# Optimization experiments

Hardware: AMD Instinct MI355X
Metric: run time of the kernel (lower is better)

The kernel has to match this reference:

```python
import jax, jax.numpy as jnp
import numpy as np

D_MODEL = 1024
N_HEADS = 16
D_K = D_MODEL // N_HEADS


def setup_inputs() -> dict:
    key = jax.random.key(0)
    ks = jax.random.split(key, 11)
    B, S = 2, 2048
    scale = 1.0 / np.sqrt(D_MODEL)
    inp = {
        "q": jax.random.normal(ks[0], (B, S, D_MODEL), jnp.float32),
        "k": jax.random.normal(ks[1], (B, S, D_MODEL), jnp.float32),
        "v": jax.random.normal(ks[2], (B, S, D_MODEL), jnp.float32),
        "W_q": jax.random.normal(ks[3], (D_MODEL, D_MODEL), jnp.float32) * scale,
        "b_q": jnp.zeros((D_MODEL,), jnp.float32),
        "W_k": jax.random.normal(ks[4], (D_MODEL, D_MODEL), jnp.float32) * scale,
        "b_k": jnp.zeros((D_MODEL,), jnp.float32),
        "W_v": jax.random.normal(ks[5], (D_MODEL, D_MODEL), jnp.float32) * scale,
        "b_v": jnp.zeros((D_MODEL,), jnp.float32),
        "W_o": jax.random.normal(ks[6], (D_MODEL, D_MODEL), jnp.float32) * scale,
        "b_o": jnp.zeros((D_MODEL,), jnp.float32),
    }
    return inp


def _split_heads(x):
    B, S, _ = x.shape
    return x.reshape(B, S, N_HEADS, D_K).transpose(0, 2, 1, 3)  # [B,H,S,dk]


def reference(q, k, v, W_q, b_q, W_k, b_k, W_v, b_v, W_o, b_o):
    Q = _split_heads(q @ W_q + b_q)
    K = _split_heads(k @ W_k + b_k)
    V = _split_heads(v @ W_v + b_v)
    scores = jnp.einsum("bhqd,bhkd->bhqk", Q, K) / jnp.sqrt(jnp.float32(D_K))
    attn = jax.nn.softmax(scores, axis=-1)  # [B,H,S,S]
    out = jnp.einsum("bhqk,bhkd->bhqd", attn, V)
    B, H, S, dk = out.shape
    out = out.transpose(0, 2, 1, 3).reshape(B, S, H * dk)
    return out @ W_o + b_o, attn
```

## Files before the change

### kernel.cpp

```cpp
#include <hip/hip_runtime.h>
#include <hip/hip_bf16.h>

typedef __bf16 bf16x8 __attribute__((ext_vector_type(8)));
typedef float f32x4 __attribute__((ext_vector_type(4)));
typedef short short4v __attribute__((ext_vector_type(4)));
typedef unsigned short ushort8v __attribute__((ext_vector_type(8)));

#define DEV static __device__ __forceinline__

#if __has_builtin(__builtin_amdgcn_exp2f)
#define EXP2(x) __builtin_amdgcn_exp2f(x)
#else
#define EXP2(x) exp2f(x)
#endif

DEV unsigned short f2bf(float x) {
  union { __hip_bfloat16 b; unsigned short u; } c;
  c.b = __float2bfloat16(x);
  return c.u;
}

DEV unsigned short f2bf_fast(float x) {
  union { float f; unsigned u; } c;
  c.f = x;
  unsigned u = c.u + 0x7fff + ((c.u >> 16) & 1);
  return (unsigned short)(u >> 16);
}

DEV void gload_lds16(const void* g, void* l) {
  __builtin_amdgcn_global_load_lds((const __attribute__((address_space(1))) void*)g,
                                   (__attribute__((address_space(3))) void*)l, 16, 0, 0);
}

__global__ __launch_bounds__(256) void cvt_qkv(const float* __restrict__ q,
                                               const float* __restrict__ k,
                                               const float* __restrict__ v,
                                               unsigned short* __restrict__ qb,
                                               unsigned short* __restrict__ kb,
                                               unsigned short* __restrict__ vb) {
  const float* src = blockIdx.y == 0 ? q : (blockIdx.y == 1 ? k : v);
  unsigned short* dst = blockIdx.y == 0 ? qb : (blockIdx.y == 1 ? kb : vb);
  int idx = (blockIdx.x * 256 + threadIdx.x) * 4;
  float4 xv = *(const float4*)(src + idx);
  ushort4 o;
  o.x = f2bf(xv.x); o.y = f2bf(xv.y); o.z = f2bf(xv.z); o.w = f2bf(xv.w);
  *(ushort4*)(dst + idx) = o;
}

__global__ __launch_bounds__(256) void transpose_all(const float* __restrict__ W0,
                                                     const float* __restrict__ W1,
                                                     const float* __restrict__ W2,
                                                     const float* __restrict__ W3,
                                                     unsigned short* __restrict__ T0,
                                                     unsigned short* __restrict__ T1,
                                                     unsigned short* __restrict__ T2,
                                                     unsigned short* __restrict__ T3) {
  __shared__ float t[64][68];
  int sel = blockIdx.x >> 8;
  const float* W = sel == 0 ? W0 : sel == 1 ? W1 : sel == 2 ? W2 : W3;
  unsigned short* Wt = sel == 0 ? T0 : sel == 1 ? T1 : sel == 2 ? T2 : T3;
  int tile = blockIdx.x & 255;
  int tr = tile >> 4, tc = tile & 15;
  int lr = threadIdx.x >> 4, lc4 = threadIdx.x & 15;
#pragma unroll
  for (int i = 0; i < 4; ++i) {
    int r = i * 16 + lr;
    float4 v = *(const float4*)(W + (size_t)(tr * 64 + r) * 1024 + tc * 64 + lc4 * 4);
    t[r][lc4 * 4 + 0] = v.x; t[r][lc4 * 4 + 1] = v.y;
    t[r][lc4 * 4 + 2] = v.z; t[r][lc4 * 4 + 3] = v.w;
  }
  __syncthreads();
#pragma unroll
  for (int i = 0; i < 4; ++i) {
    int r = i * 16 + lr;
    ushort4 o;
    o.x = f2bf(t[lc4 * 4 + 0][r]);
    o.y = f2bf(t[lc4 * 4 + 1][r]);
    o.z = f2bf(t[lc4 * 4 + 2][r]);
    o.w = f2bf(t[lc4 * 4 + 3][r]);
    *(ushort4*)(Wt + (size_t)(tc * 64 + r) * 1024 + tr * 64 + lc4 * 4) = o;
  }
}

DEV void gemm_core(const unsigned short* __restrict__ A, const unsigned short* __restrict__ Bt,
                   const float* __restrict__ bias, void* __restrict__ Cout,
                   float scale, int mode, int blk,
                   unsigned short* As, unsigned short* Bs) {
  const int tid = threadIdx.x;
  const int l = tid & 63, w = tid >> 6;
  const int wm = w >> 1, wn = w & 1;
  const int r15 = l & 15, kg = l >> 4;
  const int mt = blk >> 3, nt = blk & 7;

  const f32x4 fz = {0.f, 0.f, 0.f, 0.f};
  f32x4 acc[4][4];
#pragma unroll
  for (int i = 0; i < 4; ++i)
#pragma unroll
    for (int j = 0; j < 4; ++j) acc[i][j] = fz;

  for (int kt = 0; kt < 16; ++kt) {
#pragma unroll
    for (int c = 0; c < 4; ++c) {
      int chunk = c * 256 + tid;
      int row = chunk >> 3, slot = chunk & 7;
      int gsl = slot ^ (row & 7);
      gload_lds16(A + (size_t)(mt * 128 + row) * 1024 + kt * 64 + gsl * 8, As + chunk * 8);
      gload_lds16(Bt + (size_t)(nt * 128 + row) * 1024 + kt * 64 + gsl * 8, Bs + chunk * 8);
    }
    __syncthreads();
#pragma unroll
    for (int ks = 0; ks < 2; ++ks) {
      bf16x8 a[4], b[4];
      int slot = ks * 4 + kg;
#pragma unroll
      for (int i = 0; i < 4; ++i) {
        int ra = wm * 64 + i * 16 + r15;
        a[i] = *(const bf16x8*)(As + ra * 64 + (slot ^ (ra & 7)) * 8);
        int rb = wn * 64 + i * 16 + r15;
        b[i] = *(const bf16x8*)(Bs + rb * 64 + (slot ^ (rb & 7)) * 8);
      }
#pragma unroll
      for (int i = 0; i < 4; ++i)
#pragma unroll
        for (int j = 0; j < 4; ++j)
          acc[i][j] = __builtin_amdgcn_mfma_f32_16x16x32_bf16(a[i], b[j], acc[i][j], 0, 0, 0);
    }
    __syncthreads();
  }

#pragma unroll
  for (int j = 0; j < 4; ++j) {
    int gc = nt * 128 + wn * 64 + j * 16 + r15;
    float bj = bias[gc];
#pragma unroll
    for (int i = 0; i < 4; ++i) {
#pragma unroll
      for (int r = 0; r < 4; ++r) {
        int gr = mt * 128 + wm * 64 + i * 16 + kg * 4 + r;
        float val = (acc[i][j][r] + bj) * scale;
        if (mode == 2) {
          ((float*)Cout)[(size_t)gr * 1024 + gc] = val;
        } else {
          int bb = gr >> 11, s = gr & 2047, hh = gc >> 6, dk = gc & 63;
          if (mode == 0)
            ((unsigned short*)Cout)[((size_t)(bb * 16 + hh) * 2048 + s) * 64 + dk] = f2bf(val);
          else
            ((unsigned short*)Cout)[((size_t)(bb * 16 + hh) * 64 + dk) * 2048 + s] = f2bf(val);
        }
      }
    }
  }
}

__global__ __launch_bounds__(256) void gemm_qkv(const unsigned short* __restrict__ qb,
                                                const unsigned short* __restrict__ kb,
                                                const unsigned short* __restrict__ vb,
                                                const unsigned short* __restrict__ Wtq,
                                                const unsigned short* __restrict__ Wtk,
                                                const unsigned short* __restrict__ Wtv,
                                                const float* __restrict__ bq,
                                                const float* __restrict__ bk,
                                                const float* __restrict__ bv,
                                                unsigned short* __restrict__ Qh,
                                                unsigned short* __restrict__ Kh,
                                                unsigned short* __restrict__ Vt) {
  __shared__ unsigned short As[128 * 64];
  __shared__ unsigned short Bs[128 * 64];
  int sel = blockIdx.x >> 8, blk = blockIdx.x & 255;
  const unsigned short* A = sel == 0 ? qb : sel == 1 ? kb : vb;
  const unsigned short* Bt = sel == 0 ? Wtq : sel == 1 ? Wtk : Wtv;
  const float* bias = sel == 0 ? bq : sel == 1 ? bk : bv;
  void* C = sel == 0 ? (void*)Qh : sel == 1 ? (void*)Kh : (void*)Vt;
  gemm_core(A, Bt, bias, C, sel == 0 ? 0.125f * 1.44269504088896f : 1.0f,
            sel == 2 ? 1 : 0, blk, As, Bs);
}

__global__ __launch_bounds__(256) void gemm_out(const unsigned short* __restrict__ AO,
                                                const unsigned short* __restrict__ Wto,
                                                const float* __restrict__ bo,
                                                float* __restrict__ out0) {
  __shared__ unsigned short As[128 * 64];
  __shared__ unsigned short Bs[128 * 64];
  gemm_core(AO, Wto, bo, out0, 1.0f, 2, blockIdx.x, As, Bs);
}

__global__ __launch_bounds__(256) void attn_flash(const unsigned short* __restrict__ Qh,
                                                  const unsigned short* __restrict__ Kh,
                                                  const unsigned short* __restrict__ Vt,
                                                  unsigned short* __restrict__ AO,
                                                  float* __restrict__ rrowG) {
  __shared__ float Ored[4][32][68];
  __shared__ float Ss[4][32];
  __shared__ float rrow[32];

  const int tid = threadIdx.x;
  const int l = tid & 63, w = tid >> 6;
  const int r15 = l & 15, kg = l >> 4;

  const int lb = ((int)blockIdx.x & 7) * 256 + ((int)blockIdx.x >> 3);
  const int bh = lb >> 6;
  const int q0 = (lb & 63) * 32;
  const int b = bh >> 4, h = bh & 15;

  const unsigned short* Kbase = Kh + (size_t)bh * 2048 * 64;
  const unsigned short* Vbase = Vt + (size_t)bh * 64 * 2048;

  bf16x8 aq[2][2];
#pragma unroll
  for (int j = 0; j < 2; ++j)
#pragma unroll
    for (int h2 = 0; h2 < 2; ++h2)
      aq[j][h2] = *(const bf16x8*)(Qh + ((size_t)bh * 2048 + q0 + j * 16 + r15) * 64 +
                                   (h2 * 4 + kg) * 8);

  const f32x4 z4 = {0.f, 0.f, 0.f, 0.f};
  float s2[2] = {0.f, 0.f};
  f32x4 oacc[2][4];
#pragma unroll
  for (int j = 0; j < 2; ++j)
#pragma unroll
    for (int d = 0; d < 4; ++d) oacc[j][d] = z4;

  const int kb0 = w * 16;
  for (int kt = 0; kt < 32; ++kt) {
    const unsigned short* kp = Kbase + (size_t)(kt * 64 + kb0 + r15) * 64;
    bf16x8 kf0 = *(const bf16x8*)(kp + kg * 8);
    bf16x8 kf1 = *(const bf16x8*)(kp + 32 + kg * 8);
    short4v vf[4];
#pragma unroll
    for (int d = 0; d < 4; ++d)
      vf[d] = *(const short4v*)(Vbase + (size_t)(d * 16 + r15) * 2048 + kt * 64 + kb0 + kg * 4);
#pragma unroll
    for (int j = 0; j < 2; ++j) {
      f32x4 sc = __builtin_amdgcn_mfma_f32_16x16x32_bf16(kf0, aq[j][0], z4, 0, 0, 0);
      sc = __builtin_amdgcn_mfma_f32_16x16x32_bf16(kf1, aq[j][1], sc, 0, 0, 0);
      float e0 = EXP2(sc[0]), e1 = EXP2(sc[1]), e2 = EXP2(sc[2]), e3 = EXP2(sc[3]);
      s2[j] += (e0 + e1) + (e2 + e3);
      short4v pf;
      pf[0] = (short)f2bf_fast(e0); pf[1] = (short)f2bf_fast(e1);
      pf[2] = (short)f2bf_fast(e2); pf[3] = (short)f2bf_fast(e3);
#pragma unroll
      for (int d = 0; d < 4; ++d)
        oacc[j][d] = __builtin_amdgcn_mfma_f32_16x16x16bf16_1k(vf[d], pf, oacc[j][d], 0, 0, 0);
    }
  }

#pragma unroll
  for (int j = 0; j < 2; ++j) {
    s2[j] += __shfl_xor(s2[j], 16, 64);
    s2[j] += __shfl_xor(s2[j], 32, 64);
    if (kg == 0) Ss[w][j * 16 + r15] = s2[j];
  }
  __syncthreads();
  if (tid < 32) {
    float s = Ss[0][tid] + Ss[1][tid] + Ss[2][tid] + Ss[3][tid];
    float rv = 1.0f / s;
    rrow[tid] = rv;
    rrowG[(size_t)bh * 2048 + q0 + tid] = rv;
  }
  __syncthreads();

#pragma unroll
  for (int j = 0; j < 2; ++j)
#pragma unroll
    for (int d = 0; d < 4; ++d)
      *(f32x4*)&Ored[w][j * 16 + r15][d * 16 + kg * 4] = oacc[j][d];
  __syncthreads();
  {
    int q = tid >> 3, dc = (tid & 7) * 8;
    float rv = rrow[q];
    ushort8v o;
#pragma unroll
    for (int i = 0; i < 8; ++i) {
      float s = Ored[0][q][dc + i] + Ored[1][q][dc + i] + Ored[2][q][dc + i] + Ored[3][q][dc + i];
      o[i] = f2bf(s * rv);
    }
    *(ushort8v*)(AO + ((size_t)(b * 2048 + q0 + q)) * 1024 + h * 64 + dc) = o;
  }
}

__global__ __launch_bounds__(256) void attn_write(const unsigned short* __restrict__ Qh,
                                                  const unsigned short* __restrict__ Kh,
                                                  const float* __restrict__ rrowG,
                                                  float* __restrict__ attnO) {
  const int tid = threadIdx.x;
  const int l = tid & 63, w = tid >> 6;
  const int r15 = l & 15, kg = l >> 4;

  const int lb = ((int)blockIdx.x & 7) * 256 + ((int)blockIdx.x >> 3);
  const int bh = lb >> 6;
  const int q0 = (lb & 63) * 32;

  const unsigned short* Kbase = Kh + (size_t)bh * 2048 * 64;

  bf16x8 aq[2][2];
#pragma unroll
  for (int j = 0; j < 2; ++j)
#pragma unroll
    for (int h2 = 0; h2 < 2; ++h2)
      aq[j][h2] = *(const bf16x8*)(Qh + ((size_t)bh * 2048 + q0 + j * 16 + r15) * 64 +
                                   (h2 * 4 + kg) * 8);

  const float rvq[2] = {rrowG[(size_t)bh * 2048 + q0 + r15],
                        rrowG[(size_t)bh * 2048 + q0 + 16 + r15]};
  float* attnBase = attnO + ((size_t)bh * 2048 + q0) * 2048;
  const f32x4 z4 = {0.f, 0.f, 0.f, 0.f};

  for (int kt = 0; kt < 16; ++kt) {
    const int cb = kt * 128 + w * 32;
    const unsigned short* kp0 = Kbase + (size_t)(cb + r15) * 64;
    const unsigned short* kp1 = Kbase + (size_t)(cb + 16 + r15) * 64;
    bf16x8 kf00 = *(const bf16x8*)(kp0 + kg * 8);
    bf16x8 kf01 = *(const bf16x8*)(kp0 + 32 + kg * 8);
    bf16x8 kf10 = *(const bf16x8*)(kp1 + kg * 8);
    bf16x8 kf11 = *(const bf16x8*)(kp1 + 32 + kg * 8);
#pragma unroll
    for (int j = 0; j < 2; ++j) {
      float* rowp = attnBase + (size_t)(j * 16 + r15) * 2048 + cb + kg * 4;
      f32x4 sc = __builtin_amdgcn_mfma_f32_16x16x32_bf16(kf00, aq[j][0], z4, 0, 0, 0);
      sc = __builtin_amdgcn_mfma_f32_16x16x32_bf16(kf01, aq[j][1], sc, 0, 0, 0);
      f32x4 st0 = {EXP2(sc[0]) * rvq[j], EXP2(sc[1]) * rvq[j],
                   EXP2(sc[2]) * rvq[j], EXP2(sc[3]) * rvq[j]};
      __builtin_nontemporal_store(st0, (f32x4*)rowp);
      f32x4 sc1 = __builtin_amdgcn_mfma_f32_16x16x32_bf16(kf10, aq[j][0], z4, 0, 0, 0);
      sc1 = __builtin_amdgcn_mfma_f32_16x16x32_bf16(kf11, aq[j][1], sc1, 0, 0, 0);
      f32x4 st1 = {EXP2(sc1[0]) * rvq[j], EXP2(sc1[1]) * rvq[j],
                   EXP2(sc1[2]) * rvq[j], EXP2(sc1[3]) * rvq[j]};
      __builtin_nontemporal_store(st1, (f32x4*)(rowp + 16));
    }
  }
}

extern "C" void kernel_launch(void* const* d_in, const int* in_sizes, int n_in,
                              void* d_out, int out_size, void* d_ws, size_t ws_size,
                              hipStream_t stream) {
  const float* q  = (const float*)d_in[0];
  const float* k  = (const float*)d_in[1];
  const float* v  = (const float*)d_in[2];
  const float* Wq = (const float*)d_in[3];
  const float* bq = (const float*)d_in[4];
  const float* Wk = (const float*)d_in[5];
  const float* bk = (const float*)d_in[6];
  const float* Wv = (const float*)d_in[7];
  const float* bvp = (const float*)d_in[8];
  const float* Wo = (const float*)d_in[9];
  const float* bo = (const float*)d_in[10];

  char* wsb = (char*)d_ws;
  const size_t MB = (size_t)1 << 20;
  unsigned short* qb  = (unsigned short*)(wsb + 0 * MB);
  unsigned short* kbp = (unsigned short*)(wsb + 8 * MB);
  unsigned short* vbp = (unsigned short*)(wsb + 16 * MB);
  unsigned short* Wtq = (unsigned short*)(wsb + 24 * MB);
  unsigned short* Wtk = (unsigned short*)(wsb + 26 * MB);
  unsigned short* Wtv = (unsigned short*)(wsb + 28 * MB);
  unsigned short* Wto = (unsigned short*)(wsb + 30 * MB);
  unsigned short* Qh  = (unsigned short*)(wsb + 32 * MB);
  unsigned short* Kh  = (unsigned short*)(wsb + 40 * MB);
  unsigned short* Vt  = (unsigned short*)(wsb + 48 * MB);
  unsigned short* AO  = (unsigned short*)(wsb + 56 * MB);
  float* rrowG = (float*)(wsb + 0 * MB);

  float* attnO = (float*)d_out + (size_t)2 * 2048 * 1024;

  cvt_qkv<<<dim3(4096, 3), 256, 0, stream>>>(q, k, v, qb, kbp, vbp);
  transpose_all<<<1024, 256, 0, stream>>>(Wq, Wk, Wv, Wo, Wtq, Wtk, Wtv, Wto);
  gemm_qkv<<<768, 256, 0, stream>>>(qb, kbp, vbp, Wtq, Wtk, Wtv, bq, bk, bvp, Qh, Kh, Vt);
  attn_flash<<<2048, 256, 0, stream>>>(Qh, Kh, Vt, AO, rrowG);
  attn_write<<<2048, 256, 0, stream>>>(Qh, Kh, rrowG, attnO);
  gemm_out<<<256, 256, 0, stream>>>(AO, Wto, bo, (float*)d_out);
}
```

Before: 443.9 us.

## Restage attn_write through LDS for row-contiguous stores with double-buffered K loads

The attention-probability writer now gives each wave its own 16 query rows and stages each 16x64 score tile in padded, XOR-swizzled shared memory. Each row is then written as a contiguous 256-byte span instead of scattered 16-byte pieces per lane. K fragments are double-buffered in registers across 64-column chunks, the row scale is folded into the exponent as log2, and the grid is halved. The aim is better write coalescing on the dominant 512MB-class attn output, at the cost of extra LDS traffic and dropping the nontemporal store hints.

Result: no change. 450.4 us (+1.5%).

```diff
diff --git a/kernel.cpp b/kernel.cpp
--- a/kernel.cpp
+++ b/kernel.cpp
@@ -284,52 +284,69 @@
                                                   const unsigned short* __restrict__ Kh,
                                                   const float* __restrict__ rrowG,
                                                   float* __restrict__ attnO) {
+  __shared__ float S[4][16][72];
+
   const int tid = threadIdx.x;
   const int l = tid & 63, w = tid >> 6;
   const int r15 = l & 15, kg = l >> 4;
 
-  const int lb = ((int)blockIdx.x & 7) * 256 + ((int)blockIdx.x >> 3);
-  const int bh = lb >> 6;
-  const int q0 = (lb & 63) * 32;
+  const int lb = ((int)blockIdx.x & 7) * 128 + ((int)blockIdx.x >> 3);
+  const int bh = lb >> 5;
+  const int q0 = (lb & 31) * 64 + w * 16;
 
   const unsigned short* Kbase = Kh + (size_t)bh * 2048 * 64;
-
-  bf16x8 aq[2][2];
-#pragma unroll
-  for (int j = 0; j < 2; ++j)
-#pragma unroll
-    for (int h2 = 0; h2 < 2; ++h2)
-      aq[j][h2] = *(const bf16x8*)(Qh + ((size_t)bh * 2048 + q0 + j * 16 + r15) * 64 +
-                                   (h2 * 4 + kg) * 8);
-
-  const float rvq[2] = {rrowG[(size_t)bh * 2048 + q0 + r15],
-                        rrowG[(size_t)bh * 2048 + q0 + 16 + r15]};
+  const unsigned short* Qp = Qh + ((size_t)bh * 2048 + q0 + r15) * 64;
+  bf16x8 aq0 = *(const bf16x8*)(Qp + kg * 8);
+  bf16x8 aq1 = *(const bf16x8*)(Qp + 32 + kg * 8);
+
+  const float lrv = __log2f(rrowG[(size_t)bh * 2048 + q0 + r15]);
+
+  float* Sw = &S[w][0][0];
   float* attnBase = attnO + ((size_t)bh * 2048 + q0) * 2048;
   const f32x4 z4 = {0.f, 0.f, 0.f, 0.f};
 
-  for (int kt = 0; kt < 16; ++kt) {
-    const int cb = kt * 128 + w * 32;
-    const unsigned short* kp0 = Kbase + (size_t)(cb + r15) * 64;
-    const unsigned short* kp1 = Kbase + (size_t)(cb + 16 + r15) * 64;
-    bf16x8 kf00 = *(const bf16x8*)(kp0 + kg * 8);
-    bf16x8 kf01 = *(const bf16x8*)(kp0 + 32 + kg * 8);
-    bf16x8 kf10 = *(const bf16x8*)(kp1 + kg * 8);
-    bf16x8 kf11 = *(const bf16x8*)(kp1 + 32 + kg * 8);
-#pragma unroll
-    for (int j = 0; j < 2; ++j) {
-      float* rowp = attnBase + (size_t)(j * 16 + r15) * 2048 + cb + kg * 4;
-      f32x4 sc = __builtin_amdgcn_mfma_f32_16x16x32_bf16(kf00, aq[j][0], z4, 0, 0, 0);
-      sc = __builtin_amdgcn_mfma_f32_16x16x32_bf16(kf01, aq[j][1], sc, 0, 0, 0);
-      f32x4 st0 = {EXP2(sc[0]) * rvq[j], EXP2(sc[1]) * rvq[j],
-                   EXP2(sc[2]) * rvq[j], EXP2(sc[3]) * rvq[j]};
-      __builtin_nontemporal_store(st0, (f32x4*)rowp);
-      f32x4 sc1 = __builtin_amdgcn_mfma_f32_16x16x32_bf16(kf10, aq[j][0], z4, 0, 0, 0);
-      sc1 = __builtin_amdgcn_mfma_f32_16x16x32_bf16(kf11, aq[j][1], sc1, 0, 0, 0);
-      f32x4 st1 = {EXP2(sc1[0]) * rvq[j], EXP2(sc1[1]) * rvq[j],
-                   EXP2(sc1[2]) * rvq[j], EXP2(sc1[3]) * rvq[j]};
-      __builtin_nontemporal_store(st1, (f32x4*)(rowp + 16));
-    }
-  }
+  bf16x8 ka[4][2], kb[4][2];
+
+#define LOADK(KF, c)                                                              \
+  {                                                                               \
+    const unsigned short* kp_ = Kbase + (size_t)((c) * 64 + r15) * 64 + kg * 8;   \
+    _Pragma("unroll")                                                             \
+    for (int sub = 0; sub < 4; ++sub) {                                           \
+      KF[sub][0] = *(const bf16x8*)(kp_ + sub * 16 * 64);                         \
+      KF[sub][1] = *(const bf16x8*)(kp_ + sub * 16 * 64 + 32);                    \
+    }                                                                             \
+  }
+
+#define PROCESS(KF, c)                                                            \
+  {                                                                               \
+    _Pragma("unroll")                                                             \
+    for (int sub = 0; sub < 4; ++sub) {                                           \
+      f32x4 sc = __builtin_amdgcn_mfma_f32_16x16x32_bf16(KF[sub][0], aq0, z4, 0, 0, 0); \
+      sc = __builtin_amdgcn_mfma_f32_16x16x32_bf16(KF[sub][1], aq1, sc, 0, 0, 0); \
+      f32x4 st = {EXP2(sc[0] + lrv), EXP2(sc[1] + lrv),                           \
+                  EXP2(sc[2] + lrv), EXP2(sc[3] + lrv)};                          \
+      int col = (sub * 16 + kg * 4) ^ ((r15 & 3) << 4);                           \
+      *(f32x4*)(Sw + r15 * 72 + col) = st;                                        \
+    }                                                                             \
+    _Pragma("unroll")                                                             \
+    for (int s = 0; s < 4; ++s) {                                                 \
+      int qr = 4 * s + (l >> 4);                                                  \
+      int ci = 4 * (l & 15);                                                      \
+      int scol = ci ^ ((qr & 3) << 4);                                            \
+      f32x4 v = *(const f32x4*)(Sw + qr * 72 + scol);                             \
+      *(f32x4*)(attnBase + (size_t)qr * 2048 + (c) * 64 + ci) = v;                \
+    }                                                                             \
+  }
+
+  LOADK(ka, 0)
+  for (int c = 0; c < 32; c += 2) {
+    LOADK(kb, c + 1)
+    PROCESS(ka, c)
+    if (c + 2 < 32) LOADK(ka, c + 2)
+    PROCESS(kb, c + 1)
+  }
+#undef LOADK
+#undef PROCESS
 }
 
 extern "C" void kernel_launch(void* const* d_in, const int* in_sizes, int n_in,
@@ -368,6 +385,6 @@
   transpose_all<<<1024, 256, 0, stream>>>(Wq, Wk, Wv, Wo, Wtq, Wtk, Wtv, Wto);
   gemm_qkv<<<768, 256, 0, stream>>>(qb, kbp, vbp, Wtq, Wtk, Wtv, bq, bk, bvp, Qh, Kh, Vt);
   attn_flash<<<2048, 256, 0, stream>>>(Qh, Kh, Vt, AO, rrowG);
-  attn_write<<<2048, 256, 0, stream>>>(Qh, Kh, rrowG, attnO);
+  attn_write<<<1024, 256, 0, stream>>>(Qh, Kh, rrowG, attnO);
   gemm_out<<<256, 256, 0, stream>>>(AO, Wto, bo, (float*)d_out);
 }
```
